# Kernel optimization log

Hardware: AMD Instinct MI355X
Metric: run time of the kernel (lower is better)

## Reference

```python
import jax, jax.numpy as jnp
import numpy as np
import math

B, N, D = 4, 1024, 512
L, H, DH = 6, 8, 64
FF_INNER = 4 * D
NUM_BUCKETS, MAX_DIST = 32, 128
SCALE = 16.0  # cosine_sim_scale
ROT_DIM = 32  # min(32, dim_head)


def layernorm(x, g, stable=False, eps=1e-5):
    if stable:
        x = x / jax.lax.stop_gradient(jnp.max(x, axis=-1, keepdims=True))
    mean = jnp.mean(x, axis=-1, keepdims=True)
    var = jnp.mean(jnp.square(x - mean), axis=-1, keepdims=True)  # unbiased=False
    return (x - mean) * jax.lax.rsqrt(var + eps) * g


def l2norm(x, eps=1e-12):
    return x / jnp.maximum(jnp.linalg.norm(x, axis=-1, keepdims=True), eps)


def rotary_freqs(n):
    inv_freq = 1.0 / (10000.0 ** (jnp.arange(0, ROT_DIM, 2, dtype=jnp.float32) / ROT_DIM))
    f = jnp.arange(n, dtype=jnp.float32)[:, None] * inv_freq[None, :]  # [n, ROT_DIM/2]
    return jnp.repeat(f, 2, axis=-1)  # [n, ROT_DIM], interleaved pairs


def apply_rotary(t, freqs):
    # rotate only first ROT_DIM dims (rotary_embedding_torch semantics)
    rot, passd = t[..., :ROT_DIM], t[..., ROT_DIM:]
    x = rot.reshape(*rot.shape[:-1], ROT_DIM // 2, 2)
    rotated = jnp.stack((-x[..., 1], x[..., 0]), axis=-1).reshape(rot.shape)
    rot = rot * jnp.cos(freqs) + rotated * jnp.sin(freqs)
    return jnp.concatenate([rot, passd], axis=-1)


def rel_pos_bias(emb, i, j):
    # T5-style causal relative position buckets
    rel = jnp.arange(j)[None, :] - jnp.arange(i)[:, None]
    n = jnp.maximum(-rel, 0)
    max_exact = NUM_BUCKETS // 2
    val_large = max_exact + (
        jnp.log(jnp.maximum(n, 1).astype(jnp.float32) / max_exact)
        / math.log(MAX_DIST / max_exact) * (NUM_BUCKETS - max_exact)
    ).astype(jnp.int32)
    val_large = jnp.minimum(val_large, NUM_BUCKETS - 1)
    bucket = jnp.where(n < max_exact, n, val_large)
    return emb[bucket].transpose(2, 0, 1)  # [h, i, j]


def setup_inputs() -> dict:
    key = jax.random.key(0)
    ks = jax.random.split(key, 9)
    s = 0.02
    return {
        "x": jax.random.normal(ks[0], (B, N, D), jnp.float32),
        "rel_pos_emb": jax.random.normal(ks[1], (NUM_BUCKETS, H), jnp.float32) * s,
        "g_attn": jnp.ones((L, D), jnp.float32),
        "null_kv": jax.random.normal(ks[2], (L, 2, DH), jnp.float32),
        "Wq": jax.random.normal(ks[3], (L, D, H * DH), jnp.float32) * s,
        "Wkv": jax.random.normal(ks[4], (L, D, 2 * DH), jnp.float32) * s,
        "Wo": jax.random.normal(ks[5], (L, H * DH, D), jnp.float32) * s,
        "g_attn_out": jnp.ones((L, D), jnp.float32),
        "g_ff": jnp.ones((L, D), jnp.float32),
        "W1": jax.random.normal(ks[6], (L, D, 2 * FF_INNER), jnp.float32) * s,
        "W2": jax.random.normal(ks[7], (L, FF_INNER, D), jnp.float32) * s,
        "g_final": jnp.ones((D,), jnp.float32),
        "W_proj": jax.random.normal(ks[8], (D, D), jnp.float32) * s,
    }


def reference(x, rel_pos_emb, g_attn, null_kv, Wq, Wkv, Wo, g_attn_out, g_ff, W1, W2, g_final, W_proj):
    b, n, d = x.shape
    freqs = rotary_freqs(n)
    bias = rel_pos_bias(rel_pos_emb, n, n + 1)          # [h, n, n+1] (null kv column at j=0)
    causal = jnp.triu(jnp.ones((n, n + 1), dtype=bool), k=2)  # .triu(j - i + 1)
    neg = -jnp.finfo(x.dtype).max
    for l in range(L):
        # --- attention block ---
        xn = layernorm(x, g_attn[l])
        q = (xn @ Wq[l]).reshape(b, n, H, DH).transpose(0, 2, 1, 3) * SCALE  # b h n d
        k, v = jnp.split(xn @ Wkv[l], 2, axis=-1)                            # b n d (single-head kv)
        q = apply_rotary(q, freqs)
        k = apply_rotary(k, freqs)
        k = jnp.concatenate([jnp.broadcast_to(null_kv[l, 0], (b, 1, DH)), k], axis=1)
        v = jnp.concatenate([jnp.broadcast_to(null_kv[l, 1], (b, 1, DH)), v], axis=1)
        qn = l2norm(q) * math.sqrt(SCALE)   # cosine-sim attention
        kn = l2norm(k) * math.sqrt(SCALE)
        sim = jnp.einsum('bhid,bjd->bhij', qn, kn) + bias
        sim = jnp.where(causal, neg, sim)
        attn = jax.nn.softmax(sim.astype(jnp.float32), axis=-1).astype(x.dtype)
        o = jnp.einsum('bhij,bjd->bhid', attn, v).transpose(0, 2, 1, 3).reshape(b, n, H * DH)
        x = x + layernorm(o @ Wo[l], g_attn_out[l])
        # --- SwiGLU feedforward block ---
        hn = layernorm(x, g_ff[l])
        a, gate = jnp.split(hn @ W1[l], 2, axis=-1)
        x = x + (a * jax.nn.silu(gate)) @ W2[l]
    out = layernorm(x, g_final, stable=True)
    return out @ W_proj
```

## Files before the change

kernel.cpp:

```cpp
#include <hip/hip_runtime.h>
#include <hip/hip_bf16.h>
#include <cmath>

using bf16 = __hip_bfloat16;
typedef __bf16 v8bf __attribute__((ext_vector_type(8)));
typedef __bf16 v4bf __attribute__((ext_vector_type(4)));
typedef float  v4f  __attribute__((ext_vector_type(4)));

__device__ __forceinline__ float bf2f(bf16 x) { return __bfloat162float(x); }
__device__ __forceinline__ bf16  f2bf(float x) { return __float2bfloat16(x); }
__device__ __forceinline__ __bf16 tobf(float x) {
    bf16 h = __float2bfloat16(x);
    return __builtin_bit_cast(__bf16, h);
}

__device__ __forceinline__ void gll16(const bf16* g, bf16* l) {
    __builtin_amdgcn_global_load_lds(
        (const __attribute__((address_space(1))) unsigned int*)g,
        (__attribute__((address_space(3))) unsigned int*)l, 16, 0, 0);
}

__device__ __forceinline__ float ldin(const void* p, size_t i, int isf32) {
    if (isf32) return ((const float*)p)[i];
    return bf2f(((const bf16*)p)[i]);
}

__device__ __forceinline__ void ld8(const void* p, size_t base, int f, float v[8]) {
    if (f) {
        const float* pf = (const float*)p + base;
        float4 a = *(const float4*)pf, b = *(const float4*)(pf + 4);
        v[0]=a.x; v[1]=a.y; v[2]=a.z; v[3]=a.w;
        v[4]=b.x; v[5]=b.y; v[6]=b.z; v[7]=b.w;
    } else {
        v8bf a = *(const v8bf*)((const bf16*)p + base);
#pragma unroll
        for (int j = 0; j < 8; ++j) v[j] = (float)a[j];
    }
}

__device__ __forceinline__ float wave_sum(float v) {
#pragma unroll
    for (int o = 32; o > 0; o >>= 1) v += __shfl_xor(v, o, 64);
    return v;
}
__device__ __forceinline__ float wave_max(float v) {
#pragma unroll
    for (int o = 32; o > 0; o >>= 1) v = fmaxf(v, __shfl_xor(v, o, 64));
    return v;
}

__global__ void detect_k(const unsigned short* __restrict__ x, int* __restrict__ flag)
{
    __shared__ int s;
    int t = threadIdx.x;
    if (t == 0) s = 0;
    __syncthreads();
    int bad = 0;
    for (int i = t; i < 4096; i += 256) {
        int e = (x[i] >> 7) & 0xFF;
        if (e >= 147) bad++;
    }
    atomicAdd(&s, bad);
    __syncthreads();
    if (t == 0) *flag = (s > 64) ? 1 : 0;
}

__global__ __launch_bounds__(512, 2)
void gemm256_silu(const bf16* __restrict__ A, const bf16* __restrict__ BT,
                  bf16* __restrict__ U, int K, int lda)
{
    __shared__ bf16 As[2][256 * 64];
    __shared__ bf16 Bs[2][256 * 64];
    const int t = threadIdx.x;
    const int lane = t & 63;
    const int wave = t >> 6;
    const int wm = (wave >> 2) * 128;
    const int wn = (wave & 3) * 64;
    const int bm = blockIdx.x * 256;
    const int bn = blockIdx.y * 256;
    const int fr = lane & 15;
    const int quad = lane >> 4;

    v4f acc[8][4];
#pragma unroll
    for (int i = 0; i < 8; ++i)
#pragma unroll
        for (int j = 0; j < 4; ++j) { v4f z = {0.f, 0.f, 0.f, 0.f}; acc[i][j] = z; }

    auto stage = [&](int buf, int k0) {
#pragma unroll
        for (int r = 0; r < 4; ++r) {
            int c = t + 512 * r;
            int row = c >> 3;
            int g = (c & 7) ^ (row & 7);
            gll16(A + (size_t)(bm + row) * lda + k0 + g * 8, &As[buf][c * 8]);
            gll16(BT + (size_t)(bn + row) * K + k0 + g * 8, &Bs[buf][c * 8]);
        }
    };

    stage(0, 0);
    __syncthreads();
    const int nb = K >> 6;
    for (int kt = 0; kt < nb; ++kt) {
        const int buf = kt & 1;
        if (kt + 1 < nb) stage(buf ^ 1, (kt + 1) * 64);
#pragma unroll
        for (int ks = 0; ks < 2; ++ks) {
            v8bf af[8], bfr[4];
            const int gk = ((ks * 4 + quad) ^ (fr & 7)) * 8;
#pragma unroll
            for (int mt = 0; mt < 8; ++mt)
                af[mt] = *(const v8bf*)(&As[buf][(wm + mt * 16 + fr) * 64 + gk]);
#pragma unroll
            for (int nt = 0; nt < 4; ++nt)
                bfr[nt] = *(const v8bf*)(&Bs[buf][(wn + nt * 16 + fr) * 64 + gk]);
#pragma unroll
            for (int mt = 0; mt < 8; ++mt)
#pragma unroll
                for (int nt = 0; nt < 4; ++nt)
                    acc[mt][nt] = __builtin_amdgcn_mfma_f32_16x16x32_bf16(
                        af[mt], bfr[nt], acc[mt][nt], 0, 0, 0);
        }
        __syncthreads();
    }

    const int r0 = quad * 4;
    const int gbase = ((bn + wn) >> 6) * 32;
#pragma unroll
    for (int mt = 0; mt < 8; ++mt)
#pragma unroll
        for (int nt = 0; nt < 2; ++nt)
#pragma unroll
            for (int r = 0; r < 4; ++r) {
                int row = bm + wm + mt * 16 + r0 + r;
                int col = gbase + nt * 16 + fr;
                float a  = acc[mt][nt][r];
                float gg = acc[mt][nt + 2][r];
                U[(size_t)row * 2048 + col] = f2bf(a * (gg / (1.f + __expf(-gg))));
            }
}


__global__ __launch_bounds__(256)
void gemm64(const bf16* __restrict__ A, const bf16* __restrict__ BT,
            bf16* __restrict__ C, int M, int N, int K, int lda)
{
    __shared__ bf16 As[64 * 32];
    __shared__ bf16 Bs[128 * 32];
    const int t = threadIdx.x;
    const int lane = t & 63;
    const int wave = t >> 6;
    const int wm = (wave >> 1) * 32;
    const int wn = (wave & 1) * 64;
    const int bm = blockIdx.x * 64;
    const int bn = blockIdx.y * 128;
    const int fr = lane & 15;
    const int fk = (((lane >> 4) ^ ((fr >> 1) & 3))) * 8;

    v4f acc[2][4];
#pragma unroll
    for (int i = 0; i < 2; ++i)
#pragma unroll
        for (int j = 0; j < 4; ++j) { v4f z = {0.f, 0.f, 0.f, 0.f}; acc[i][j] = z; }

    for (int k0 = 0; k0 < K; k0 += 32) {
        {
            int row = t >> 2;
            int koff = ((t & 3) ^ ((row >> 1) & 3)) * 8;
            gll16(A + (size_t)(bm + row) * lda + k0 + koff, &As[t * 8]);
        }
#pragma unroll
        for (int r = 0; r < 2; ++r) {
            int c = t + 256 * r;
            int row = c >> 2;
            int koff = ((c & 3) ^ ((row >> 1) & 3)) * 8;
            gll16(BT + (size_t)(bn + row) * K + k0 + koff, &Bs[c * 8]);
        }
        __syncthreads();
        v8bf af[2], bfr[4];
#pragma unroll
        for (int mt = 0; mt < 2; ++mt)
            af[mt] = *(const v8bf*)(&As[(wm + mt * 16 + fr) * 32 + fk]);
#pragma unroll
        for (int nt = 0; nt < 4; ++nt)
            bfr[nt] = *(const v8bf*)(&Bs[(wn + nt * 16 + fr) * 32 + fk]);
#pragma unroll
        for (int mt = 0; mt < 2; ++mt)
#pragma unroll
            for (int nt = 0; nt < 4; ++nt)
                acc[mt][nt] = __builtin_amdgcn_mfma_f32_16x16x32_bf16(
                    af[mt], bfr[nt], acc[mt][nt], 0, 0, 0);
        __syncthreads();
    }
    const int r0 = (lane >> 4) * 4;
#pragma unroll
    for (int mt = 0; mt < 2; ++mt)
#pragma unroll
        for (int nt = 0; nt < 4; ++nt)
#pragma unroll
            for (int r = 0; r < 4; ++r) {
                int row = bm + wm + mt * 16 + r0 + r;
                int col = bn + wn + nt * 16 + fr;
                C[(size_t)row * N + col] = f2bf(acc[mt][nt][r]);
            }
}

__global__ __launch_bounds__(256)
void gemm64_out(const bf16* __restrict__ A, const bf16* __restrict__ BT,
                void* __restrict__ C, int M, int N, int K, int lda,
                const int* __restrict__ flag)
{
    __shared__ bf16 As[64 * 32];
    __shared__ bf16 Bs[128 * 32];
    const int f = *flag;
    const int t = threadIdx.x;
    const int lane = t & 63;
    const int wave = t >> 6;
    const int wm = (wave >> 1) * 32;
    const int wn = (wave & 1) * 64;
    const int bm = blockIdx.x * 64;
    const int bn = blockIdx.y * 128;
    const int fr = lane & 15;
    const int fk = (((lane >> 4) ^ ((fr >> 1) & 3))) * 8;

    v4f acc[2][4];
#pragma unroll
    for (int i = 0; i < 2; ++i)
#pragma unroll
        for (int j = 0; j < 4; ++j) { v4f z = {0.f, 0.f, 0.f, 0.f}; acc[i][j] = z; }

    for (int k0 = 0; k0 < K; k0 += 32) {
        {
            int row = t >> 2;
            int koff = ((t & 3) ^ ((row >> 1) & 3)) * 8;
            gll16(A + (size_t)(bm + row) * lda + k0 + koff, &As[t * 8]);
        }
#pragma unroll
        for (int r = 0; r < 2; ++r) {
            int c = t + 256 * r;
            int row = c >> 2;
            int koff = ((c & 3) ^ ((row >> 1) & 3)) * 8;
            gll16(BT + (size_t)(bn + row) * K + k0 + koff, &Bs[c * 8]);
        }
        __syncthreads();
        v8bf af[2], bfr[4];
#pragma unroll
        for (int mt = 0; mt < 2; ++mt)
            af[mt] = *(const v8bf*)(&As[(wm + mt * 16 + fr) * 32 + fk]);
#pragma unroll
        for (int nt = 0; nt < 4; ++nt)
            bfr[nt] = *(const v8bf*)(&Bs[(wn + nt * 16 + fr) * 32 + fk]);
#pragma unroll
        for (int mt = 0; mt < 2; ++mt)
#pragma unroll
            for (int nt = 0; nt < 4; ++nt)
                acc[mt][nt] = __builtin_amdgcn_mfma_f32_16x16x32_bf16(
                    af[mt], bfr[nt], acc[mt][nt], 0, 0, 0);
        __syncthreads();
    }
    const int r0 = (lane >> 4) * 4;
#pragma unroll
    for (int mt = 0; mt < 2; ++mt)
#pragma unroll
        for (int nt = 0; nt < 4; ++nt)
#pragma unroll
            for (int r = 0; r < 4; ++r) {
                int row = bm + wm + mt * 16 + r0 + r;
                int col = bn + wn + nt * 16 + fr;
                if (f) ((float*)C)[(size_t)row * N + col] = acc[mt][nt][r];
                else   ((bf16*)C)[(size_t)row * N + col] = f2bf(acc[mt][nt][r]);
            }
}

__global__ __launch_bounds__(256)
void transpose2_k(const void* __restrict__ in, bf16* __restrict__ out, int R, int C,
                  size_t inZ, size_t outZ, const int* __restrict__ flag)
{
    __shared__ bf16 tile[32][33];
    int f = *flag;
    size_t ioff = (size_t)blockIdx.z * inZ;
    bf16* dst = out + (size_t)blockIdx.z * outZ;
    int c0 = blockIdx.x * 32, r0 = blockIdx.y * 32;
    int tx = threadIdx.x, ty = threadIdx.y;
#pragma unroll
    for (int i = 0; i < 32; i += 8)
        tile[ty + i][tx] = f2bf(ldin(in, ioff + (size_t)(r0 + ty + i) * C + c0 + tx, f));
    __syncthreads();
#pragma unroll
    for (int i = 0; i < 32; i += 8)
        dst[(size_t)(c0 + ty + i) * R + r0 + tx] = tile[tx][ty + i];
}

__global__ __launch_bounds__(256)
void transposeW1_k(const void* __restrict__ in, bf16* __restrict__ out,
                   const int* __restrict__ flag)
{
    __shared__ bf16 tile[32][33];
    int f = *flag;
    size_t ioff = (size_t)blockIdx.z * (512ull * 4096);
    bf16* dst = out + (size_t)blockIdx.z * (512ull * 4096);
    int c0 = blockIdx.x * 32, r0 = blockIdx.y * 32;
    int tx = threadIdx.x, ty = threadIdx.y;
#pragma unroll
    for (int i = 0; i < 32; i += 8)
        tile[ty + i][tx] = f2bf(ldin(in, ioff + (size_t)(r0 + ty + i) * 4096 + c0 + tx, f));
    __syncthreads();
#pragma unroll
    for (int i = 0; i < 32; i += 8) {
        int j = c0 + ty + i;
        int jp = (j < 2048) ? (((j >> 5) << 6) | (j & 31))
                            : ((((j - 2048) >> 5) << 6) | 32 | (j & 31));
        dst[(size_t)jp * 512 + r0 + tx] = tile[tx][ty + i];
    }
}

__global__ __launch_bounds__(256)
void xinit_ln_k(const void* __restrict__ in, const void* __restrict__ g,
                const int* __restrict__ flag, float* __restrict__ x, bf16* __restrict__ xn)
{
    int f = *flag;
    int row = blockIdx.x * 4 + (threadIdx.x >> 6);
    int lane = threadIdx.x & 63;
    int c0 = lane * 8;
    float v[8];
    ld8(in, (size_t)row * 512 + c0, f, v);
    float* xr = x + (size_t)row * 512 + c0;
    *(float4*)xr       = make_float4(v[0], v[1], v[2], v[3]);
    *(float4*)(xr + 4) = make_float4(v[4], v[5], v[6], v[7]);
    float s = 0.f;
#pragma unroll
    for (int j = 0; j < 8; ++j) s += v[j];
    float mean = wave_sum(s) * (1.f / 512.f);
    float q = 0.f;
#pragma unroll
    for (int j = 0; j < 8; ++j) { float d = v[j] - mean; q += d * d; }
    float var = wave_sum(q) * (1.f / 512.f);
    float rstd = rsqrtf(var + 1e-5f);
    float gv[8];
    ld8(g, c0, f, gv);
    v8bf o;
#pragma unroll
    for (int j = 0; j < 8; ++j) o[j] = tobf((v[j] - mean) * rstd * gv[j]);
    *(v8bf*)(xn + (size_t)row * 512 + c0) = o;
}

__global__ __launch_bounds__(256)
void addln_ln_k(const bf16* __restrict__ tin, const void* __restrict__ g1, int g1off,
                const void* __restrict__ g2, int g2off, const int* __restrict__ flag,
                float* __restrict__ x, bf16* __restrict__ xn)
{
    int f = *flag;
    int row = blockIdx.x * 4 + (threadIdx.x >> 6);
    int lane = threadIdx.x & 63;
    int c0 = lane * 8;
    float tv[8];
    {
        v8bf a = *(const v8bf*)(tin + (size_t)row * 512 + c0);
#pragma unroll
        for (int j = 0; j < 8; ++j) tv[j] = (float)a[j];
    }
    float s = 0.f;
#pragma unroll
    for (int j = 0; j < 8; ++j) s += tv[j];
    float mean = wave_sum(s) * (1.f / 512.f);
    float q = 0.f;
#pragma unroll
    for (int j = 0; j < 8; ++j) { float d = tv[j] - mean; q += d * d; }
    float var = wave_sum(q) * (1.f / 512.f);
    float rstd = rsqrtf(var + 1e-5f);
    float g1v[8];
    ld8(g1, (size_t)g1off + c0, f, g1v);
    float* xr = x + (size_t)row * 512 + c0;
    float4 xa = *(float4*)xr, xb = *(float4*)(xr + 4);
    float nx[8] = {xa.x, xa.y, xa.z, xa.w, xb.x, xb.y, xb.z, xb.w};
#pragma unroll
    for (int j = 0; j < 8; ++j) nx[j] += (tv[j] - mean) * rstd * g1v[j];
    *(float4*)xr       = make_float4(nx[0], nx[1], nx[2], nx[3]);
    *(float4*)(xr + 4) = make_float4(nx[4], nx[5], nx[6], nx[7]);
    float s2 = 0.f;
#pragma unroll
    for (int j = 0; j < 8; ++j) s2 += nx[j];
    float mean2 = wave_sum(s2) * (1.f / 512.f);
    float q2 = 0.f;
#pragma unroll
    for (int j = 0; j < 8; ++j) { float e = nx[j] - mean2; q2 += e * e; }
    float var2 = wave_sum(q2) * (1.f / 512.f);
    float rstd2 = rsqrtf(var2 + 1e-5f);
    float g2v[8];
    ld8(g2, (size_t)g2off + c0, f, g2v);
    v8bf o;
#pragma unroll
    for (int j = 0; j < 8; ++j) o[j] = tobf((nx[j] - mean2) * rstd2 * g2v[j]);
    *(v8bf*)(xn + (size_t)row * 512 + c0) = o;
}

__global__ __launch_bounds__(256)
void add_ln_k(const bf16* __restrict__ tin, const void* __restrict__ g, int goff,
              const int* __restrict__ flag, int stable,
              float* __restrict__ x, bf16* __restrict__ xn)
{
    int f = *flag;
    int row = blockIdx.x * 4 + (threadIdx.x >> 6);
    int lane = threadIdx.x & 63;
    int c0 = lane * 8;
    float nx[8];
    {
        v8bf a = *(const v8bf*)(tin + (size_t)row * 512 + c0);
        float* xr = x + (size_t)row * 512 + c0;
        float4 xa = *(float4*)xr, xb = *(float4*)(xr + 4);
        float xv[8] = {xa.x, xa.y, xa.z, xa.w, xb.x, xb.y, xb.z, xb.w};
#pragma unroll
        for (int j = 0; j < 8; ++j) nx[j] = xv[j] + (float)a[j];
        *(float4*)xr       = make_float4(nx[0], nx[1], nx[2], nx[3]);
        *(float4*)(xr + 4) = make_float4(nx[4], nx[5], nx[6], nx[7]);
    }
    float v[8];
#pragma unroll
    for (int j = 0; j < 8; ++j) v[j] = nx[j];
    if (stable) {
        float m = v[0];
#pragma unroll
        for (int j = 1; j < 8; ++j) m = fmaxf(m, v[j]);
        float mx = wave_max(m);
#pragma unroll
        for (int j = 0; j < 8; ++j) v[j] /= mx;
    }
    float s = 0.f;
#pragma unroll
    for (int j = 0; j < 8; ++j) s += v[j];
    float mean = wave_sum(s) * (1.f / 512.f);
    float q = 0.f;
#pragma unroll
    for (int j = 0; j < 8; ++j) { float d = v[j] - mean; q += d * d; }
    float var = wave_sum(q) * (1.f / 512.f);
    float rstd = rsqrtf(var + 1e-5f);
    float gv[8];
    ld8(g, (size_t)goff + c0, f, gv);
    v8bf o;
#pragma unroll
    for (int j = 0; j < 8; ++j) o[j] = tobf((v[j] - mean) * rstd * gv[j]);
    *(v8bf*)(xn + (size_t)row * 512 + c0) = o;
}

__global__ __launch_bounds__(256)
void rotab_k(float2* __restrict__ tab)
{
    int idx = blockIdx.x * 256 + threadIdx.x;
    if (idx >= 16384) return;
    int n = idx >> 4, p = idx & 15;
    float ang = (float)n * expf((float)p * -0.5756462732f);
    tab[idx] = make_float2(cosf(ang), sinf(ang));
}

__global__ __launch_bounds__(256)
void bias_k(const void* __restrict__ rpe, const int* __restrict__ flag, float* __restrict__ tab)
{
    int f = *flag;
    int idx = blockIdx.x * 256 + threadIdx.x;
    if (idx >= 8 * 1025) return;
    int h = idx / 1025, dist = idx % 1025;
    int bkt;
    if (dist < 16) bkt = dist;
    else {
        bkt = 16 + (int)(logf((float)dist / 16.f) / logf(8.f) * 16.f);
        if (bkt > 31) bkt = 31;
    }
    tab[idx] = ldin(rpe, bkt * 8 + h, f) - 16.f;
}

__global__ __launch_bounds__(256)
void qkvprep_k(const bf16* __restrict__ qkv, const void* __restrict__ nkv, int nkoff,
               const int* __restrict__ flag, const float2* __restrict__ rtab,
               bf16* __restrict__ Q, bf16* __restrict__ K, bf16* __restrict__ Vt)
{
    int t = threadIdx.x, lane = t & 63;
    int bid = blockIdx.x;
    if (bid < 2048) {
        int rid = bid * 16 + (t >> 4);
        int h = rid & 7;
        int n = (rid >> 3) & 1023;
        int b = rid >> 13;
        int g16 = t & 15;
        int d0 = g16 * 4;
        v4bf a = *(const v4bf*)(qkv + (size_t)((b << 10) | n) * 640 + h * 64 + d0);
        float v[4];
#pragma unroll
        for (int j = 0; j < 4; ++j) v[j] = (float)a[j] * 16.f;
        if (d0 < 32) {
            float4 cs = *(const float4*)((const float*)rtab + (size_t)n * 32 + (size_t)(d0 >> 1) * 2);
            float r0 = v[0] * cs.x - v[1] * cs.y;
            float r1 = v[1] * cs.x + v[0] * cs.y;
            float r2 = v[2] * cs.z - v[3] * cs.w;
            float r3 = v[3] * cs.z + v[2] * cs.w;
            v[0] = r0; v[1] = r1; v[2] = r2; v[3] = r3;
        }
        float ss = v[0]*v[0] + v[1]*v[1] + v[2]*v[2] + v[3]*v[3];
#pragma unroll
        for (int o = 1; o < 16; o <<= 1) ss += __shfl_xor(ss, o, 64);
        float sc = 4.f / fmaxf(sqrtf(ss), 1e-12f);
        v4bf ov;
#pragma unroll
        for (int j = 0; j < 4; ++j) ov[j] = tobf(v[j] * sc);
        *(v4bf*)(Q + (((size_t)(b * 8 + h)) * 1024 + n) * 64 + d0) = ov;
    } else {
        int f = *flag;
        int rid = (bid - 2048) * 4 + (t >> 6);
        if (rid >= 4 * 1088) return;
        int j = rid % 1088;
        int b = rid / 1088;
        if (j >= 1025) {
            K[((size_t)b * 1088 + j) * 64 + lane] = f2bf(0.f);
            Vt[((size_t)b * 64 + lane) * 1088 + j] = f2bf(0.f);
            return;
        }
        float kv, vv;
        if (j == 0) {
            kv = ldin(nkv, nkoff + lane, f);
            vv = ldin(nkv, nkoff + 64 + lane, f);
        } else {
            int n = j - 1;
            const bf16* src = qkv + (size_t)(b * 1024 + n) * 640 + 512;
            kv = bf2f(src[lane]);
            vv = bf2f(src[64 + lane]);
            if (lane < 32) {
                float2 cs = rtab[n * 16 + (lane >> 1)];
                float other = __shfl_xor(kv, 1, 64);
                float rot = (lane & 1) ? other : -other;
                kv = kv * cs.x + rot * cs.y;
            }
        }
        float nrm = sqrtf(wave_sum(kv * kv));
        kv = kv / fmaxf(nrm, 1e-12f) * 4.f;
        K[((size_t)b * 1088 + j) * 64 + lane] = f2bf(kv);
        Vt[((size_t)b * 64 + lane) * 1088 + j] = f2bf(vv);
    }
}

__global__ __launch_bounds__(256)
void attn_mfma(const bf16* __restrict__ Q, const bf16* __restrict__ Kg,
               const bf16* __restrict__ Vtg, const float* __restrict__ bias,
               bf16* __restrict__ O)
{
    __shared__ bf16 Ks[64][72];
    __shared__ bf16 Vts[64][72];
    __shared__ bf16 Ps[4][16][72];
    __shared__ float bs[1088];
    const int bh = blockIdx.x, b = bh >> 3, h = bh & 7;
    const int yy = (int)gridDim.y - 1 - (int)blockIdx.y;
    const int i0 = yy * 64;
    const int t = threadIdx.x, lane = t & 63, w = t >> 6;
    const int col = lane & 15, quad = lane >> 4, fk = quad * 8;
    const float* bt = bias + h * 1025;
    const bf16* Kb = Kg + (size_t)b * 1088 * 64;
    const bf16* Vb = Vtg + (size_t)b * 64 * 1088;

    for (int idx = t; idx < i0 + 64; idx += 256) bs[idx] = bt[idx];

    v8bf qf[2];
    const bf16* qrow = Q + ((size_t)bh * 1024 + i0 + w * 16 + col) * 64;
    qf[0] = *(const v8bf*)(qrow + fk);
    qf[1] = *(const v8bf*)(qrow + 32 + fk);

    v4f oacc[4];
#pragma unroll
    for (int dt = 0; dt < 4; ++dt) { v4f z = {0.f,0.f,0.f,0.f}; oacc[dt] = z; }
    float lpart[4] = {0.f, 0.f, 0.f, 0.f};

    const int nch = yy + 2;
    const int rr0 = t >> 3, co0 = (t & 7) * 8;
    const int rr1 = (t + 256) >> 3, co1 = co0;

    v8bf kr[2], vr[2];
    {
        kr[0] = *(const v8bf*)(Kb + (size_t)rr0 * 64 + co0);
        vr[0] = *(const v8bf*)(Vb + (size_t)rr0 * 1088 + co0);
        kr[1] = *(const v8bf*)(Kb + (size_t)rr1 * 64 + co1);
        vr[1] = *(const v8bf*)(Vb + (size_t)rr1 * 1088 + co1);
    }

    for (int ch = 0; ch < nch; ++ch) {
        const int j0 = ch * 64;
        __syncthreads();
        *(v8bf*)(&Ks[rr0][co0])  = kr[0];
        *(v8bf*)(&Vts[rr0][co0]) = vr[0];
        *(v8bf*)(&Ks[rr1][co1])  = kr[1];
        *(v8bf*)(&Vts[rr1][co1]) = vr[1];
        if (ch + 1 < nch) {
            int j0n = (ch + 1) * 64;
            kr[0] = *(const v8bf*)(Kb + (size_t)(j0n + rr0) * 64 + co0);
            vr[0] = *(const v8bf*)(Vb + (size_t)rr0 * 1088 + j0n + co0);
            kr[1] = *(const v8bf*)(Kb + (size_t)(j0n + rr1) * 64 + co1);
            vr[1] = *(const v8bf*)(Vb + (size_t)rr1 * 1088 + j0n + co1);
        }
        __syncthreads();

        v4f sreg[4];
#pragma unroll
        for (int nt = 0; nt < 4; ++nt) {
            v4f z = {0.f,0.f,0.f,0.f};
            v8bf kf0 = *(const v8bf*)(&Ks[nt * 16 + col][fk]);
            v8bf kf1 = *(const v8bf*)(&Ks[nt * 16 + col][32 + fk]);
            z = __builtin_amdgcn_mfma_f32_16x16x32_bf16(qf[0], kf0, z, 0, 0, 0);
            z = __builtin_amdgcn_mfma_f32_16x16x32_bf16(qf[1], kf1, z, 0, 0, 0);
            sreg[nt] = z;
        }

        if (ch < yy) {
#pragma unroll
            for (int reg = 0; reg < 4; ++reg) {
                int i = i0 + w * 16 + quad * 4 + reg;
                int dbase = i - j0 - col;
#pragma unroll
                for (int nt = 0; nt < 4; ++nt) {
                    float pp = __expf(sreg[nt][reg] + bs[dbase - nt * 16]);
                    lpart[reg] += pp;
                    Ps[w][quad * 4 + reg][nt * 16 + col] = f2bf(pp);
                }
            }
        } else {
#pragma unroll
            for (int reg = 0; reg < 4; ++reg) {
                int i = i0 + w * 16 + quad * 4 + reg;
#pragma unroll
                for (int nt = 0; nt < 4; ++nt) {
                    int j = j0 + nt * 16 + col;
                    float pp = 0.f;
                    if (j <= i + 1 && j < 1025) {
                        int dist = i - j; if (dist < 0) dist = 0;
                        pp = __expf(sreg[nt][reg] + bs[dist]);
                    }
                    lpart[reg] += pp;
                    Ps[w][quad * 4 + reg][nt * 16 + col] = f2bf(pp);
                }
            }
        }

        v8bf pf[2];
        pf[0] = *(const v8bf*)(&Ps[w][col][fk]);
        pf[1] = *(const v8bf*)(&Ps[w][col][32 + fk]);
#pragma unroll
        for (int dt = 0; dt < 4; ++dt) {
#pragma unroll
            for (int ks = 0; ks < 2; ++ks) {
                v8bf vf = *(const v8bf*)(&Vts[dt * 16 + col][ks * 32 + fk]);
                oacc[dt] = __builtin_amdgcn_mfma_f32_16x16x32_bf16(pf[ks], vf, oacc[dt], 0, 0, 0);
            }
        }
    }

#pragma unroll
    for (int reg = 0; reg < 4; ++reg) {
#pragma unroll
        for (int o = 1; o < 16; o <<= 1) lpart[reg] += __shfl_xor(lpart[reg], o, 64);
        float inv = 1.f / lpart[reg];
        int i = i0 + w * 16 + quad * 4 + reg;
        bf16* orow = O + ((size_t)(b * 1024 + i)) * 512 + h * 64;
#pragma unroll
        for (int dt = 0; dt < 4; ++dt)
            orow[dt * 16 + col] = f2bf(oacc[dt][reg] * inv);
    }
}

extern "C" void kernel_launch(void* const* d_in, const int* in_sizes, int n_in,
                              void* d_out, int out_size, void* d_ws, size_t ws_size,
                              hipStream_t stream)
{
    const void* x_in     = d_in[0];
    const void* rpe      = d_in[1];
    const void* g_attn   = d_in[2];
    const void* null_kv  = d_in[3];
    const void* Wq       = d_in[4];
    const void* Wkv      = d_in[5];
    const void* Wo       = d_in[6];
    const void* g_attn_o = d_in[7];
    const void* g_ff     = d_in[8];
    const void* W1       = d_in[9];
    const void* W2       = d_in[10];
    const void* g_final  = d_in[11];
    const void* W_proj   = d_in[12];

    char* wp = (char*)d_ws;
    auto alloc = [&](size_t bytes) {
        char* p = wp; wp += (bytes + 255) & ~(size_t)255; return p;
    };
    float* xf    = (float*)alloc(4096ull * 512 * 4);
    bf16*  xn    = (bf16*) alloc(4096ull * 512 * 2);
    bf16*  tb    = (bf16*) alloc(4096ull * 512 * 2);
    bf16*  ub    = (bf16*) alloc(4096ull * 4096 * 2);
    bf16*  Kb    = (bf16*) alloc(4ull * 1088 * 64 * 2);
    bf16*  Vtb   = (bf16*) alloc(4ull * 64 * 1088 * 2);
    float* btab  = (float*)alloc(8ull * 1025 * 4);
    float2* rtab = (float2*)alloc(16384ull * 8);
    int*   dfl   = (int*)  alloc(256);
    bf16*  WqkvT = (bf16*) alloc(6ull * 640 * 512 * 2);
    bf16*  WoT   = (bf16*) alloc(6ull * 512 * 512 * 2);
    bf16*  W1T   = (bf16*) alloc(6ull * 4096 * 512 * 2);
    bf16*  W2T   = (bf16*) alloc(6ull * 512 * 2048 * 2);
    bf16*  WpT   = (bf16*) alloc(512ull * 512 * 2);
    bf16*  qkvb  = ub;
    bf16*  Qb    = ub + 2621440;
    bf16*  ob    = ub + 4718592;

    detect_k<<<1, 256, 0, stream>>>((const unsigned short*)x_in, dfl);
    transpose2_k<<<dim3(16, 16, 6),  dim3(32, 8), 0, stream>>>(Wq, WqkvT, 512, 512, 512ull*512, 640ull*512, dfl);
    transpose2_k<<<dim3(4, 16, 6),   dim3(32, 8), 0, stream>>>(Wkv, WqkvT + 512ull*512, 512, 128, 512ull*128, 640ull*512, dfl);
    transpose2_k<<<dim3(16, 16, 6),  dim3(32, 8), 0, stream>>>(Wo, WoT, 512, 512, 512ull*512, 512ull*512, dfl);
    transposeW1_k<<<dim3(128, 16, 6), dim3(32, 8), 0, stream>>>(W1, W1T, dfl);
    transpose2_k<<<dim3(16, 64, 6),  dim3(32, 8), 0, stream>>>(W2, W2T, 2048, 512, 2048ull*512, 2048ull*512, dfl);
    transpose2_k<<<dim3(16, 16, 1),  dim3(32, 8), 0, stream>>>(W_proj, WpT, 512, 512, 512ull*512, 512ull*512, dfl);
    bias_k<<<33, 256, 0, stream>>>(rpe, dfl, btab);
    rotab_k<<<64, 256, 0, stream>>>(rtab);
    xinit_ln_k<<<1024, 256, 0, stream>>>(x_in, g_attn, dfl, xf, xn);

    for (int l = 0; l < 6; ++l) {
        gemm64<<<dim3(64, 5), 256, 0, stream>>>(xn, WqkvT + (size_t)l * 640 * 512, qkvb, 4096, 640, 512, 512);
        qkvprep_k<<<3136, 256, 0, stream>>>(qkvb, null_kv, l * 128, dfl, rtab, Qb, Kb, Vtb);
        attn_mfma<<<dim3(32, 16), 256, 0, stream>>>(Qb, Kb, Vtb, btab, ob);
        gemm64<<<dim3(64, 4), 256, 0, stream>>>(ob, WoT + (size_t)l * 512 * 512, tb, 4096, 512, 512, 512);
        addln_ln_k<<<1024, 256, 0, stream>>>(tb, g_attn_o, l * 512, g_ff, l * 512, dfl, xf, xn);
        gemm256_silu<<<dim3(16, 16), 512, 0, stream>>>(xn, W1T + (size_t)l * 4096 * 512, ub, 512, 512);
        gemm64<<<dim3(64, 4), 256, 0, stream>>>(ub, W2T + (size_t)l * 512 * 2048, tb, 4096, 512, 2048, 2048);
        if (l < 5)
            add_ln_k<<<1024, 256, 0, stream>>>(tb, g_attn, (l + 1) * 512, dfl, 0, xf, xn);
        else
            add_ln_k<<<1024, 256, 0, stream>>>(tb, g_final, 0, dfl, 1, xf, xn);
    }
    gemm64_out<<<dim3(64, 4), 256, 0, stream>>>(xn, WpT, d_out, 4096, 512, 512, 512, dfl);
}
```

Before: 896.0 us.

## Double-buffer LDS and widen K-tile to 64 in gemm64 kernels

The 64x128 GEMM kernels now use two LDS buffers with a 64-wide K tile. Each iteration prefetches the next tile through global_load_lds while MFMAs run on the current one, and a single barrier per iteration replaces two. The LDS swizzle is changed to an 8-group XOR to match the wider rows. This quadruples shared memory per block, which may reduce occupancy, and it assumes K is a multiple of 64.

```diff
diff --git a/kernel.cpp b/kernel.cpp
--- a/kernel.cpp
+++ b/kernel.cpp
@@ -140,13 +140,12 @@
             }
 }
 
-
 __global__ __launch_bounds__(256)
 void gemm64(const bf16* __restrict__ A, const bf16* __restrict__ BT,
             bf16* __restrict__ C, int M, int N, int K, int lda)
 {
-    __shared__ bf16 As[64 * 32];
-    __shared__ bf16 Bs[128 * 32];
+    __shared__ bf16 As[2][64 * 64];
+    __shared__ bf16 Bs[2][128 * 64];
     const int t = threadIdx.x;
     const int lane = t & 63;
     const int wave = t >> 6;
@@ -155,7 +154,7 @@
     const int bm = blockIdx.x * 64;
     const int bn = blockIdx.y * 128;
     const int fr = lane & 15;
-    const int fk = (((lane >> 4) ^ ((fr >> 1) & 3))) * 8;
+    const int quad = lane >> 4;
 
     v4f acc[2][4];
 #pragma unroll
@@ -163,36 +162,49 @@
 #pragma unroll
         for (int j = 0; j < 4; ++j) { v4f z = {0.f, 0.f, 0.f, 0.f}; acc[i][j] = z; }
 
-    for (int k0 = 0; k0 < K; k0 += 32) {
-        {
-            int row = t >> 2;
-            int koff = ((t & 3) ^ ((row >> 1) & 3)) * 8;
-            gll16(A + (size_t)(bm + row) * lda + k0 + koff, &As[t * 8]);
-        }
+    auto stage = [&](int buf, int k0) {
 #pragma unroll
         for (int r = 0; r < 2; ++r) {
             int c = t + 256 * r;
-            int row = c >> 2;
-            int koff = ((c & 3) ^ ((row >> 1) & 3)) * 8;
-            gll16(BT + (size_t)(bn + row) * K + k0 + koff, &Bs[c * 8]);
+            int row = c >> 3;
+            int g = (c & 7) ^ (row & 7);
+            gll16(A + (size_t)(bm + row) * lda + k0 + g * 8, &As[buf][c * 8]);
+        }
+#pragma unroll
+        for (int r = 0; r < 4; ++r) {
+            int c = t + 256 * r;
+            int row = c >> 3;
+            int g = (c & 7) ^ (row & 7);
+            gll16(BT + (size_t)(bn + row) * K + k0 + g * 8, &Bs[buf][c * 8]);
+        }
+    };
+
+    stage(0, 0);
+    __syncthreads();
+    const int nb = K >> 6;
+    for (int kt = 0; kt < nb; ++kt) {
+        const int buf = kt & 1;
+        if (kt + 1 < nb) stage(buf ^ 1, (kt + 1) * 64);
+#pragma unroll
+        for (int ks = 0; ks < 2; ++ks) {
+            v8bf af[2], bfr[4];
+            const int gk = ((ks * 4 + quad) ^ (fr & 7)) * 8;
+#pragma unroll
+            for (int mt = 0; mt < 2; ++mt)
+                af[mt] = *(const v8bf*)(&As[buf][(wm + mt * 16 + fr) * 64 + gk]);
+#pragma unroll
+            for (int nt = 0; nt < 4; ++nt)
+                bfr[nt] = *(const v8bf*)(&Bs[buf][(wn + nt * 16 + fr) * 64 + gk]);
+#pragma unroll
+            for (int mt = 0; mt < 2; ++mt)
+#pragma unroll
+                for (int nt = 0; nt < 4; ++nt)
+                    acc[mt][nt] = __builtin_amdgcn_mfma_f32_16x16x32_bf16(
+                        af[mt], bfr[nt], acc[mt][nt], 0, 0, 0);
         }
         __syncthreads();
-        v8bf af[2], bfr[4];
-#pragma unroll
-        for (int mt = 0; mt < 2; ++mt)
-            af[mt] = *(const v8bf*)(&As[(wm + mt * 16 + fr) * 32 + fk]);
-#pragma unroll
-        for (int nt = 0; nt < 4; ++nt)
-            bfr[nt] = *(const v8bf*)(&Bs[(wn + nt * 16 + fr) * 32 + fk]);
-#pragma unroll
-        for (int mt = 0; mt < 2; ++mt)
-#pragma unroll
-            for (int nt = 0; nt < 4; ++nt)
-                acc[mt][nt] = __builtin_amdgcn_mfma_f32_16x16x32_bf16(
-                    af[mt], bfr[nt], acc[mt][nt], 0, 0, 0);
-        __syncthreads();
-    }
-    const int r0 = (lane >> 4) * 4;
+    }
+    const int r0 = quad * 4;
 #pragma unroll
     for (int mt = 0; mt < 2; ++mt)
 #pragma unroll
@@ -210,8 +222,8 @@
                 void* __restrict__ C, int M, int N, int K, int lda,
                 const int* __restrict__ flag)
 {
-    __shared__ bf16 As[64 * 32];
-    __shared__ bf16 Bs[128 * 32];
+    __shared__ bf16 As[2][64 * 64];
+    __shared__ bf16 Bs[2][128 * 64];
     const int f = *flag;
     const int t = threadIdx.x;
     const int lane = t & 63;
@@ -221,7 +233,7 @@
     const int bm = blockIdx.x * 64;
     const int bn = blockIdx.y * 128;
     const int fr = lane & 15;
-    const int fk = (((lane >> 4) ^ ((fr >> 1) & 3))) * 8;
+    const int quad = lane >> 4;
 
     v4f acc[2][4];
 #pragma unroll
@@ -229,36 +241,49 @@
 #pragma unroll
         for (int j = 0; j < 4; ++j) { v4f z = {0.f, 0.f, 0.f, 0.f}; acc[i][j] = z; }
 
-    for (int k0 = 0; k0 < K; k0 += 32) {
-        {
-            int row = t >> 2;
-            int koff = ((t & 3) ^ ((row >> 1) & 3)) * 8;
-            gll16(A + (size_t)(bm + row) * lda + k0 + koff, &As[t * 8]);
-        }
+    auto stage = [&](int buf, int k0) {
 #pragma unroll
         for (int r = 0; r < 2; ++r) {
             int c = t + 256 * r;
-            int row = c >> 2;
-            int koff = ((c & 3) ^ ((row >> 1) & 3)) * 8;
-            gll16(BT + (size_t)(bn + row) * K + k0 + koff, &Bs[c * 8]);
+            int row = c >> 3;
+            int g = (c & 7) ^ (row & 7);
+            gll16(A + (size_t)(bm + row) * lda + k0 + g * 8, &As[buf][c * 8]);
+        }
+#pragma unroll
+        for (int r = 0; r < 4; ++r) {
+            int c = t + 256 * r;
+            int row = c >> 3;
+            int g = (c & 7) ^ (row & 7);
+            gll16(BT + (size_t)(bn + row) * K + k0 + g * 8, &Bs[buf][c * 8]);
+        }
+    };
+
+    stage(0, 0);
+    __syncthreads();
+    const int nb = K >> 6;
+    for (int kt = 0; kt < nb; ++kt) {
+        const int buf = kt & 1;
+        if (kt + 1 < nb) stage(buf ^ 1, (kt + 1) * 64);
+#pragma unroll
+        for (int ks = 0; ks < 2; ++ks) {
+            v8bf af[2], bfr[4];
+            const int gk = ((ks * 4 + quad) ^ (fr & 7)) * 8;
+#pragma unroll
+            for (int mt = 0; mt < 2; ++mt)
+                af[mt] = *(const v8bf*)(&As[buf][(wm + mt * 16 + fr) * 64 + gk]);
+#pragma unroll
+            for (int nt = 0; nt < 4; ++nt)
+                bfr[nt] = *(const v8bf*)(&Bs[buf][(wn + nt * 16 + fr) * 64 + gk]);
+#pragma unroll
+            for (int mt = 0; mt < 2; ++mt)
+#pragma unroll
+                for (int nt = 0; nt < 4; ++nt)
+                    acc[mt][nt] = __builtin_amdgcn_mfma_f32_16x16x32_bf16(
+                        af[mt], bfr[nt], acc[mt][nt], 0, 0, 0);
         }
         __syncthreads();
-        v8bf af[2], bfr[4];
-#pragma unroll
-        for (int mt = 0; mt < 2; ++mt)
-            af[mt] = *(const v8bf*)(&As[(wm + mt * 16 + fr) * 32 + fk]);
-#pragma unroll
-        for (int nt = 0; nt < 4; ++nt)
-            bfr[nt] = *(const v8bf*)(&Bs[(wn + nt * 16 + fr) * 32 + fk]);
-#pragma unroll
-        for (int mt = 0; mt < 2; ++mt)
-#pragma unroll
-            for (int nt = 0; nt < 4; ++nt)
-                acc[mt][nt] = __builtin_amdgcn_mfma_f32_16x16x32_bf16(
-                    af[mt], bfr[nt], acc[mt][nt], 0, 0, 0);
-        __syncthreads();
-    }
-    const int r0 = (lane >> 4) * 4;
+    }
+    const int r0 = quad * 4;
 #pragma unroll
     for (int mt = 0; mt < 2; ++mt)
 #pragma unroll
```

Result: faster. 852.2 us (-4.9%).
